# Kernel optimization log

Measured on AMD Instinct MI355X. Metric: run time of the kernel, lower is better.

Reference implementation:

```python
import jax, jax.numpy as jnp
import numpy as np

K = 5            # local_window_size
S = K * K + 1    # num_affinity_samples = 26


def _local_indices(H, W, k):
    # Mirrors generate_local_indices: reflection-pad an arange index map and
    # unfold kxk windows -> [H*W, k*k] flat node indices.
    p = (k - 1) // 2
    idx = np.arange(H * W, dtype=np.int64).reshape(H, W)
    idx = np.pad(idx, p, mode='reflect')
    win = np.lib.stride_tricks.sliding_window_view(idx, (k, k))  # [H,W,k,k]
    return win.reshape(H * W, k * k)


def setup_inputs() -> dict:
    key = jax.random.key(0)
    ks = jax.random.split(key, 8)
    B, C, H, W = 4, 64, 128, 128
    D = 64  # kq_dim
    s = 1.0 / np.sqrt(C)
    return {
        'x': jax.random.normal(ks[0], (B, C, H, W), jnp.float32),
        'conv_w': jax.random.normal(ks[1], (D, C), jnp.float32) * s,
        'conv_b': jax.random.normal(ks[2], (D,), jnp.float32) * 0.01,
        'key_w': jax.random.normal(ks[3], (D, D), jnp.float32) * s,
        'key_b': jax.random.normal(ks[4], (D,), jnp.float32) * 0.01,
        'query_w': jax.random.normal(ks[5], (D, D), jnp.float32) * s,
        'query_b': jax.random.normal(ks[6], (D,), jnp.float32) * 0.01,
        'rand_global_inds': jax.random.randint(ks[7], (B, H * W, S - K * K), 0, H * W).astype(jnp.int64),
    }


def reference(x, conv_w, conv_b, key_w, key_b, query_w, query_b, rand_global_inds):
    B, C, H, W = x.shape
    HW = H * W
    # 1x1 conv (kq_conv): [B,C,H,W] -> [B,H,W,D]
    kq = jnp.einsum('bchw,dc->bhwd', x, conv_w) + conv_b
    # keys/query decoders (torch Linear: y = x W^T + b), flattened to [B,HW,D]
    keys = (kq @ key_w.T + key_b).reshape(B, HW, -1)
    queries = (kq @ query_w.T + query_b).reshape(B, HW, -1)
    # sample indices: 25 local window neighbors + 1 random global per node
    local = jnp.asarray(_local_indices(H, W, K))                 # [HW, 25]
    local = jnp.broadcast_to(local[None], (B, HW, K * K))
    sample_inds = jnp.concatenate([local, rand_global_inds], -1)  # [B,HW,S]
    # gather keys at sampled indices: [B,HW,S,D]
    gathered_key = jax.vmap(lambda k, idx: k[idx])(keys, sample_inds)
    # per-sample dot product with the node's own query, scaled by C^-0.5
    logits = jnp.einsum('bnd,bnsd->bns', queries, gathered_key) * (C ** -0.5)
    return logits
```

## Files before the change

### kernel.cpp

```cpp
#include <hip/hip_runtime.h>
#include <hip/hip_bf16.h>

#define HW 16384
#define NB 4

typedef __attribute__((ext_vector_type(8))) short bf16x8;
typedef __attribute__((ext_vector_type(4))) float f32x4;

__device__ __forceinline__ float blo(unsigned u) { return __uint_as_float(u << 16); }
__device__ __forceinline__ float bhi(unsigned u) { return __uint_as_float(u & 0xffff0000u); }

__device__ __forceinline__ float bdot(unsigned k, unsigned q, float c) {
#if __has_builtin(__builtin_amdgcn_fdot2_f32_bf16)
    typedef __attribute__((ext_vector_type(2))) __bf16 bf16x2;
    return __builtin_amdgcn_fdot2_f32_bf16(__builtin_bit_cast(bf16x2, k),
                                           __builtin_bit_cast(bf16x2, q), c, false);
#else
    return fmaf(blo(k), blo(q), fmaf(bhi(k), bhi(q), c));
#endif
}


__global__ __launch_bounds__(256) void combine_weights(
    const float* __restrict__ conv_w, const float* __restrict__ conv_b,
    const float* __restrict__ key_w, const float* __restrict__ key_b,
    const float* __restrict__ query_w, const float* __restrict__ query_b,
    ushort* __restrict__ Wb, float* __restrict__ bout) {
    int t = threadIdx.x, bx = blockIdx.x;
    int sel = bx >> 4, d0 = (bx & 15) * 4;
    const float* Wm = sel ? query_w : key_w;
    float scale = sel ? 0.125f : 1.0f;
    int dd = t >> 6, c = t & 63;
    const float* wrow = Wm + (d0 + dd) * 64;
    float acc = 0.f;
    #pragma unroll
    for (int k = 0; k < 64; ++k) acc = fmaf(wrow[k], conv_w[k * 64 + c], acc);
    __hip_bfloat16 h = __float2bfloat16(acc * scale);
    Wb[(sel * 64 + d0 + dd) * 64 + c] = *(ushort*)&h;
    if (t < 4) {
        const float* wr2 = Wm + (d0 + t) * 64;
        float bacc = 0.f;
        #pragma unroll
        for (int k = 0; k < 64; ++k) bacc = fmaf(wr2[k], conv_b[k], bacc);
        bacc += (sel ? query_b : key_b)[d0 + t];
        bout[sel * 64 + d0 + t] = bacc * scale;
    }
}

__global__ __launch_bounds__(256) void gemm_kq(
    const float* __restrict__ x, const ushort* __restrict__ W,
    const float* __restrict__ bias, ushort* __restrict__ keys,
    ushort* __restrict__ queries) {
    __shared__ ushort xs[128 * 64];
    __shared__ ushort epi[2 * 128 * 64];
    __shared__ float bs[128];
    int t = threadIdx.x;
    int b = blockIdx.x >> 7;
    int n0 = (blockIdx.x & 127) << 7;

    if (t < 128) bs[t] = bias[t];
    {
        int c0 = (t >> 5) * 8, nb = (t & 31) * 4;
        const float* xp = x + ((size_t)(b * 64 + c0)) * HW + n0 + nb;
        float4 v[8];
        #pragma unroll
        for (int r = 0; r < 8; ++r) v[r] = *(const float4*)(xp + (size_t)r * HW);
        int chunk = c0 >> 3;
        #pragma unroll
        for (int nn = 0; nn < 4; ++nn) {
            unsigned u[4];
            #pragma unroll
            for (int cc = 0; cc < 4; ++cc) {
                float lo = ((const float*)&v[2 * cc])[nn];
                float hi = ((const float*)&v[2 * cc + 1])[nn];
                __hip_bfloat162 h2 = __float22bfloat162_rn(make_float2(lo, hi));
                u[cc] = *(unsigned*)&h2;
            }
            int row = nb + nn;
            *(uint4*)((char*)xs + row * 128 + ((chunk ^ (row & 7)) << 4)) =
                make_uint4(u[0], u[1], u[2], u[3]);
        }
    }
    __syncthreads();

    int l = t & 63, w = t >> 6;
    int ncol = l & 15, kg = l >> 4;
    int nhalf = w & 1, dhalf = w >> 1;

    bf16x8 Bf[4][2];
    #pragma unroll
    for (int nt = 0; nt < 4; ++nt) {
        int row = nhalf * 64 + nt * 16 + ncol;
        #pragma unroll
        for (int half = 0; half < 2; ++half)
            Bf[nt][half] = *(bf16x8*)((char*)xs + row * 128 + (((half * 4 + kg) ^ (row & 7)) << 4));
    }

    f32x4 acc[4][4];
    #pragma unroll
    for (int dt = 0; dt < 4; ++dt)
        #pragma unroll
        for (int nt = 0; nt < 4; ++nt) acc[dt][nt] = (f32x4){0.f, 0.f, 0.f, 0.f};

    #pragma unroll
    for (int dt = 0; dt < 4; ++dt) {
        const bf16x8* arow = (const bf16x8*)(W + ((dhalf * 64 + dt * 16 + ncol)) * 64 + kg * 8);
        bf16x8 A0 = arow[0];
        bf16x8 A1 = arow[4];
        #pragma unroll
        for (int nt = 0; nt < 4; ++nt) {
            acc[dt][nt] = __builtin_amdgcn_mfma_f32_16x16x32_bf16(A0, Bf[nt][0], acc[dt][nt], 0, 0, 0);
            acc[dt][nt] = __builtin_amdgcn_mfma_f32_16x16x32_bf16(A1, Bf[nt][1], acc[dt][nt], 0, 0, 0);
        }
    }

    #pragma unroll
    for (int dt = 0; dt < 4; ++dt) {
        int dbase = dt * 16 + kg * 4;
        float4 bb = *(float4*)&bs[dhalf * 64 + dbase];
        #pragma unroll
        for (int nt = 0; nt < 4; ++nt) {
            int nl = nhalf * 64 + nt * 16 + ncol;
            f32x4 a = acc[dt][nt];
            __hip_bfloat162 lo2 = __float22bfloat162_rn(make_float2(a[0] + bb.x, a[1] + bb.y));
            __hip_bfloat162 hi2 = __float22bfloat162_rn(make_float2(a[2] + bb.z, a[3] + bb.w));
            *(uint2*)((char*)epi + dhalf * 16384 + nl * 128 +
                      (((dbase >> 3) ^ (nl & 7)) << 4) + ((dbase & 4) << 1)) =
                make_uint2(*(unsigned*)&lo2, *(unsigned*)&hi2);
        }
    }
    __syncthreads();
    #pragma unroll
    for (int i = 0; i < 8; ++i) {
        int u = i * 256 + t;
        int arr = u >> 10;
        int row = (u >> 3) & 127, ch = u & 7;
        uint4 v = *(uint4*)((char*)epi + arr * 16384 + row * 128 + ((ch ^ (row & 7)) << 4));
        ushort* dst = arr ? queries : keys;
        *(uint4*)(dst + (((size_t)(b * HW + n0 + row)) << 6) + ch * 8) = v;
    }
}

#define DOT(s_, idxn_) do {                                                   \
    const uint4* kp = (const uint4*)(kb_ + ((size_t)(idxn_) << 6));           \
    uint4 ka = kp[0], kc = kp[1];                                             \
    float a0, a1;                                                             \
    a0 = bdot(ka.x, qa.x, 0.f);                                               \
    a0 = bdot(ka.y, qa.y, a0);                                                \
    a0 = bdot(ka.z, qa.z, a0);                                                \
    a0 = bdot(ka.w, qa.w, a0);                                                \
    a1 = bdot(kc.x, qb.x, 0.f);                                               \
    a1 = bdot(kc.y, qb.y, a1);                                                \
    a1 = bdot(kc.z, qb.z, a1);                                                \
    a1 = bdot(kc.w, qb.w, a1);                                                \
    float a = a0 + a1;                                                        \
    a += __shfl_xor(a, 1);                                                    \
    a += __shfl_xor(a, 2);                                                    \
    if (j == 0) res[n_loc * 26 + (s_)] = a;                                   \
} while (0)

#define SAMP(s_, dy_, dx_) do {                                               \
    int ry = y + (dy_);                                                       \
    if ((dy_) < 0) ry = (ry < 0) ? -ry : ry;                                  \
    if ((dy_) > 0) ry = (ry > 127) ? 254 - ry : ry;                           \
    int rx = xq + (dx_);                                                      \
    if ((dx_) < 0) rx = (rx < 0) ? -rx : rx;                                  \
    if ((dx_) > 0) rx = (rx > 127) ? 254 - rx : rx;                           \
    DOT(s_, (ry << 7) + rx);                                                  \
} while (0)

__global__ __launch_bounds__(256) void affinity(
    const ushort* __restrict__ keys, const ushort* __restrict__ queries,
    const int* __restrict__ rnd, float* __restrict__ out) {
    __shared__ float res[416];
    int t = threadIdx.x;
    int b = blockIdx.x >> 10;
    int n0 = (blockIdx.x & 1023) << 4;

    int j = t & 3;
    int g = t >> 2;
    int n_loc = g & 15;
    int sb = g >> 4;
    int n = n0 + n_loc;

    const uint4* qp = (const uint4*)(queries + (((size_t)(b * HW + n)) << 6) + j * 16);
    uint4 qa = qp[0], qb = qp[1];

    int y = n >> 7, xq = n & 127;
    const ushort* kb_ = keys + (((size_t)b * HW) << 6) + j * 16;

    switch (sb) {
    case 0:
        SAMP(0, -2, -2); SAMP(4, -2, 2);  SAMP(8, -1, 1);  SAMP(12, 0, 0);
        SAMP(16, 1, -1); SAMP(20, 2, -2); SAMP(24, 2, 2);
        break;
    case 1: {
        SAMP(1, -2, -1); SAMP(5, -1, -2); SAMP(9, -1, 2);  SAMP(13, 0, 1);
        SAMP(17, 1, 0);  SAMP(21, 2, -1);
        int rix = rnd[b * HW + n];
        DOT(25, rix);
        break;
    }
    case 2:
        SAMP(2, -2, 0);  SAMP(6, -1, -1); SAMP(10, 0, -2); SAMP(14, 0, 2);
        SAMP(18, 1, 1);  SAMP(22, 2, 0);
        break;
    default:
        SAMP(3, -2, 1);  SAMP(7, -1, 0);  SAMP(11, 0, -1); SAMP(15, 1, -2);
        SAMP(19, 1, 2);  SAMP(23, 2, 1);
        break;
    }
    __syncthreads();
    size_t ob = ((size_t)(b * HW + n0)) * 26;
    out[ob + t] = res[t];
    if (t < 160) out[ob + 256 + t] = res[256 + t];
}

extern "C" void kernel_launch(void* const* d_in, const int* in_sizes, int n_in,
                              void* d_out, int out_size, void* d_ws, size_t ws_size,
                              hipStream_t stream) {
    const float* x       = (const float*)d_in[0];
    const float* conv_w  = (const float*)d_in[1];
    const float* conv_b  = (const float*)d_in[2];
    const float* key_w   = (const float*)d_in[3];
    const float* key_b   = (const float*)d_in[4];
    const float* query_w = (const float*)d_in[5];
    const float* query_b = (const float*)d_in[6];
    const int*   rnd     = (const int*)d_in[7];
    float* out = (float*)d_out;

    ushort* Wb    = (ushort*)d_ws;
    float*  biasp = (float*)((char*)d_ws + 16384);
    ushort* keys  = (ushort*)((char*)d_ws + 32768);
    ushort* quer  = keys + (size_t)NB * HW * 64;

    combine_weights<<<32, 256, 0, stream>>>(conv_w, conv_b, key_w, key_b,
                                            query_w, query_b, Wb, biasp);
    gemm_kq<<<NB * (HW / 128), 256, 0, stream>>>(x, Wb, biasp, keys, quer);
    affinity<<<NB * (HW / 16), 256, 0, stream>>>(keys, quer, rnd, out);
}
```

Before: 34.24 us.

## Stage 5x68 key halo tile in LDS for local-window affinity

The affinity kernel now handles 64 consecutive pixels of one row per block. It first loads a 5-row by 68-column reflected key halo into swizzled shared memory, then computes all 25 local dot products from LDS, and only the random global sample still reads from global memory. This replaces 25 scattered global/L2 key reads per pixel with a shared staging load reused about 25 times. The cost is about 43KB of LDS per block, which may limit occupancy, plus a barrier after staging and a quarter as many blocks.

```diff
diff --git a/kernel.cpp b/kernel.cpp
--- a/kernel.cpp
+++ b/kernel.cpp
@@ -18,6 +18,10 @@
 #else
     return fmaf(blo(k), blo(q), fmaf(bhi(k), bhi(q), c));
 #endif
+}
+
+__device__ __forceinline__ int refl(int i) {
+    return i < 0 ? -i : (i > 127 ? 254 - i : i);
 }
 
 
@@ -141,9 +145,13 @@
     }
 }
 
-#define DOT(s_, idxn_) do {                                                   \
-    const uint4* kp = (const uint4*)(kb_ + ((size_t)(idxn_) << 6));           \
-    uint4 ka = kp[0], kc = kp[1];                                             \
+
+#define LSAMP(s_, dy_, dx_) do {                                              \
+    int lrow = l2 + ((dy_) + 2) * 68 + (dx_);                                 \
+    uint4 ka = *(const uint4*)((char*)klds + lrow * 128 +                     \
+                               (((2 * j) ^ (lrow & 7)) << 4));                \
+    uint4 kc = *(const uint4*)((char*)klds + lrow * 128 +                     \
+                               (((2 * j + 1) ^ (lrow & 7)) << 4));            \
     float a0, a1;                                                             \
     a0 = bdot(ka.x, qa.x, 0.f);                                               \
     a0 = bdot(ka.y, qa.y, a0);                                                \
@@ -156,64 +164,76 @@
     float a = a0 + a1;                                                        \
     a += __shfl_xor(a, 1);                                                    \
     a += __shfl_xor(a, 2);                                                    \
-    if (j == 0) res[n_loc * 26 + (s_)] = a;                                   \
-} while (0)
-
-#define SAMP(s_, dy_, dx_) do {                                               \
-    int ry = y + (dy_);                                                       \
-    if ((dy_) < 0) ry = (ry < 0) ? -ry : ry;                                  \
-    if ((dy_) > 0) ry = (ry > 127) ? 254 - ry : ry;                           \
-    int rx = xq + (dx_);                                                      \
-    if ((dx_) < 0) rx = (rx < 0) ? -rx : rx;                                  \
-    if ((dx_) > 0) rx = (rx > 127) ? 254 - rx : rx;                           \
-    DOT(s_, (ry << 7) + rx);                                                  \
+    if (j == 0) res[l * 26 + (s_)] = a;                                       \
 } while (0)
 
 __global__ __launch_bounds__(256) void affinity(
     const ushort* __restrict__ keys, const ushort* __restrict__ queries,
     const int* __restrict__ rnd, float* __restrict__ out) {
-    __shared__ float res[416];
+    __shared__ ushort klds[340 * 64];
+    __shared__ float res[64 * 26];
     int t = threadIdx.x;
-    int b = blockIdx.x >> 10;
-    int n0 = (blockIdx.x & 1023) << 4;
+    int bid = blockIdx.x;
+    int b = bid >> 8;
+    int rem = bid & 255;
+    int y = rem >> 1;
+    int x0 = (rem & 1) << 6;
+    int n0 = (y << 7) + x0;
+
+    const ushort* kbase = keys + (((size_t)b * HW) << 6);
+
+    for (int u = t; u < 2720; u += 256) {
+        int srow = u >> 3, chunk = u & 7;
+        int r = srow / 68, c = srow - r * 68;
+        int yy = refl(y + r - 2);
+        int xx = refl(x0 + c - 2);
+        uint4 v = *(const uint4*)(kbase + (((size_t)((yy << 7) + xx)) << 6) + chunk * 8);
+        *(uint4*)((char*)klds + srow * 128 + ((chunk ^ (srow & 7)) << 4)) = v;
+    }
 
     int j = t & 3;
-    int g = t >> 2;
-    int n_loc = g & 15;
-    int sb = g >> 4;
-    int n = n0 + n_loc;
+    int l = t >> 2;
+    int l2 = l + 2;
+    int n = n0 + l;
 
     const uint4* qp = (const uint4*)(queries + (((size_t)(b * HW + n)) << 6) + j * 16);
     uint4 qa = qp[0], qb = qp[1];
-
-    int y = n >> 7, xq = n & 127;
-    const ushort* kb_ = keys + (((size_t)b * HW) << 6) + j * 16;
-
-    switch (sb) {
-    case 0:
-        SAMP(0, -2, -2); SAMP(4, -2, 2);  SAMP(8, -1, 1);  SAMP(12, 0, 0);
-        SAMP(16, 1, -1); SAMP(20, 2, -2); SAMP(24, 2, 2);
-        break;
-    case 1: {
-        SAMP(1, -2, -1); SAMP(5, -1, -2); SAMP(9, -1, 2);  SAMP(13, 0, 1);
-        SAMP(17, 1, 0);  SAMP(21, 2, -1);
-        int rix = rnd[b * HW + n];
-        DOT(25, rix);
-        break;
-    }
-    case 2:
-        SAMP(2, -2, 0);  SAMP(6, -1, -1); SAMP(10, 0, -2); SAMP(14, 0, 2);
-        SAMP(18, 1, 1);  SAMP(22, 2, 0);
-        break;
-    default:
-        SAMP(3, -2, 1);  SAMP(7, -1, 0);  SAMP(11, 0, -1); SAMP(15, 1, -2);
-        SAMP(19, 1, 2);  SAMP(23, 2, 1);
-        break;
-    }
+    int rix = rnd[b * HW + n];
+    __syncthreads();
+
+    LSAMP(0, -2, -2);  LSAMP(1, -2, -1);  LSAMP(2, -2, 0);   LSAMP(3, -2, 1);
+    LSAMP(4, -2, 2);   LSAMP(5, -1, -2);  LSAMP(6, -1, -1);  LSAMP(7, -1, 0);
+    LSAMP(8, -1, 1);   LSAMP(9, -1, 2);   LSAMP(10, 0, -2);  LSAMP(11, 0, -1);
+    LSAMP(12, 0, 0);   LSAMP(13, 0, 1);   LSAMP(14, 0, 2);   LSAMP(15, 1, -2);
+    LSAMP(16, 1, -1);  LSAMP(17, 1, 0);   LSAMP(18, 1, 1);   LSAMP(19, 1, 2);
+    LSAMP(20, 2, -2);  LSAMP(21, 2, -1);  LSAMP(22, 2, 0);   LSAMP(23, 2, 1);
+    LSAMP(24, 2, 2);
+
+    {
+        const uint4* kp = (const uint4*)(kbase + ((size_t)rix << 6) + j * 16);
+        uint4 ka = kp[0], kc = kp[1];
+        float a0, a1;
+        a0 = bdot(ka.x, qa.x, 0.f);
+        a0 = bdot(ka.y, qa.y, a0);
+        a0 = bdot(ka.z, qa.z, a0);
+        a0 = bdot(ka.w, qa.w, a0);
+        a1 = bdot(kc.x, qb.x, 0.f);
+        a1 = bdot(kc.y, qb.y, a1);
+        a1 = bdot(kc.z, qb.z, a1);
+        a1 = bdot(kc.w, qb.w, a1);
+        float a = a0 + a1;
+        a += __shfl_xor(a, 1);
+        a += __shfl_xor(a, 2);
+        if (j == 0) res[l * 26 + 25] = a;
+    }
+
     __syncthreads();
     size_t ob = ((size_t)(b * HW + n0)) * 26;
-    out[ob + t] = res[t];
-    if (t < 160) out[ob + 256 + t] = res[256 + t];
+    #pragma unroll
+    for (int i = 0; i < 7; ++i) {
+        int idx = i * 256 + t;
+        if (idx < 1664) out[ob + idx] = res[idx];
+    }
 }
 
 extern "C" void kernel_launch(void* const* d_in, const int* in_sizes, int n_in,
@@ -237,5 +257,5 @@
     combine_weights<<<32, 256, 0, stream>>>(conv_w, conv_b, key_w, key_b,
                                             query_w, query_b, Wb, biasp);
     gemm_kq<<<NB * (HW / 128), 256, 0, stream>>>(x, Wb, biasp, keys, quer);
-    affinity<<<NB * (HW / 16), 256, 0, stream>>>(keys, quer, rnd, out);
-}
+    affinity<<<NB * (HW / 16) / 4, 256, 0, stream>>>(keys, quer, rnd, out);
+}
```

Result: slower. 42.58 us (+24.4%).
